# Performance work log

Hardware: AMD Instinct MI355X
Metric: run time of the kernel (lower is better)

Reference implementation:

```python
import jax, jax.numpy as jnp
import numpy as np

THRESHOLD = 0.5
EPS = 1e-8


def cos_sim(a, b):
    # a: [M, D], b: [N, D] -> [M, N] cosine similarity
    a_n = jnp.linalg.norm(a, axis=1, keepdims=True)
    b_n = jnp.linalg.norm(b, axis=1, keepdims=True)
    a_norm = a / jnp.maximum(a_n, EPS)
    b_norm = b / jnp.maximum(b_n, EPS)
    return a_norm @ b_norm.T


def setup_inputs() -> dict:
    key = jax.random.key(0)
    k1, k2, k3, k4 = jax.random.split(key, 4)
    N1, N2, FEA_FT, W_FT = 8192, 8192, 128, 64
    fea1 = jax.random.normal(k1, (N1, FEA_FT), dtype=jnp.float32)
    fea2 = jax.random.normal(k2, (N2, FEA_FT), dtype=jnp.float32)
    # xavier_uniform with relu gain sqrt(2): limit = gain * sqrt(6/(fan_in+fan_out))
    gain = float(np.sqrt(2.0))
    limit = gain * float(np.sqrt(6.0 / (FEA_FT + W_FT)))
    w1 = jax.random.uniform(k3, (FEA_FT, W_FT), minval=-limit, maxval=limit, dtype=jnp.float32)
    w2 = jax.random.uniform(k4, (FEA_FT, W_FT), minval=-limit, maxval=limit, dtype=jnp.float32)
    return {"fea1": fea1, "fea2": fea2, "w1": w1, "w2": w2}


def reference(fea1, fea2, w1, w2):
    embed1 = fea1 @ w1  # [N1, w_ft]
    embed2 = fea2 @ w2  # [N2, w_ft]
    sim_up = cos_sim(embed1, embed2)  # [N1, N2]
    sims_up = jnp.where(sim_up < THRESHOLD, jnp.zeros_like(sim_up), sim_up)
    sim_uu = cos_sim(embed1, embed1)  # [N1, N1]
    sims_uu = jnp.where(sim_uu < THRESHOLD, jnp.zeros_like(sim_uu), sim_uu)
    # Edge lists in the original are nonzero(sims_up)/nonzero(sims_uu); we return
    # the thresholded similarity matrices (jit-safe, fixed shape), stacked.
    return jnp.stack([sims_up, sims_uu], axis=0)  # [2, N, N]
```

## Files before the change

kernel.cpp:

```cpp
#include <hip/hip_runtime.h>

#define THRESH 0.5f
#define BAND   1e-3f

constexpr int N  = 8192;
constexpr int FD = 128;
constexpr int WD = 64;

typedef __attribute__((ext_vector_type(8)))  short short8;
typedef __attribute__((ext_vector_type(4)))  float f32x4;

static __device__ __forceinline__ unsigned short f2bf(float x) {
  union { float f; unsigned u; } v; v.f = x;
  unsigned r = v.u + 0x7FFFu + ((v.u >> 16) & 1u);
  return (unsigned short)(r >> 16);
}
static __device__ __forceinline__ float bf2f(unsigned short h) {
  union { unsigned u; float f; } v; v.u = (unsigned)h << 16;
  return v.f;
}

static __device__ __noinline__ float exact_dot(const float* __restrict__ a,
                                               const float* __restrict__ b) {
  float s = 0.f;
#pragma unroll 1
  for (int k = 0; k < WD; ++k) s = fmaf(a[k], b[k], s);
  return s;
}

__global__ __launch_bounds__(256) void embed_norm(
    const float* __restrict__ fea1, const float* __restrict__ fea2,
    const float* __restrict__ w1,   const float* __restrict__ w2,
    float* __restrict__ E1n, float* __restrict__ E2n,
    unsigned short* __restrict__ E1h, unsigned short* __restrict__ E1l,
    unsigned short* __restrict__ E2h, unsigned short* __restrict__ E2l) {
  const int which = blockIdx.y;
  const float* __restrict__ fea = which ? fea2 : fea1;
  const float* __restrict__ w   = which ? w2   : w1;
  float*          En = which ? E2n : E1n;
  unsigned short* Eh = which ? E2h : E1h;
  unsigned short* El = which ? E2l : E1l;

  __shared__ float wl[FD * WD];
  __shared__ float fl[32][FD];

  const int t    = threadIdx.x;
  const int row0 = blockIdx.x * 32;

#pragma unroll
  for (int i = 0; i < 8; ++i) {
    const int idx = (t + i * 256) * 4;
    *(float4*)&wl[idx] = *(const float4*)&w[idx];
  }
#pragma unroll
  for (int i = 0; i < 4; ++i) {
    const int idx = t + i * 256;
    const int r = idx >> 5;
    const int c = (idx & 31) * 4;
    *(float4*)&fl[r][c] = *(const float4*)&fea[(size_t)(row0 + r) * FD + c];
  }
  __syncthreads();

  const int wave = t >> 6, lane = t & 63;
#pragma unroll 1
  for (int rr = 0; rr < 8; ++rr) {
    const int r = wave * 8 + rr;
    float acc = 0.f;
#pragma unroll 16
    for (int k = 0; k < FD; ++k)
      acc = fmaf(fl[r][k], wl[k * WD + lane], acc);
    float ss = acc * acc;
#pragma unroll
    for (int m = 32; m >= 1; m >>= 1) ss += __shfl_xor(ss, m, 64);
    const float scale = 1.f / fmaxf(sqrtf(ss), 1e-8f);
    const float e = acc * scale;
    const size_t o = (size_t)(row0 + r) * WD + lane;
    En[o] = e;
    const unsigned short h = f2bf(e);
    Eh[o] = h;
    El[o] = f2bf(e - bf2f(h));
  }
}

__global__ __launch_bounds__(256) void sim_mfma(
    const unsigned short* __restrict__ E1h, const unsigned short* __restrict__ E1l,
    const unsigned short* __restrict__ E2h, const unsigned short* __restrict__ E2l,
    const float* __restrict__ E1n, const float* __restrict__ E2n,
    float* __restrict__ out) {
  const int bi = blockIdx.y, bj = blockIdx.x;
  const int t = threadIdx.x, w = t >> 6, lane = t & 63;
  const int wr = w >> 1, wc = w & 1;
  const int row0 = bi * 128 + wr * 64;
  const int col0 = bj * 128 + wc * 64;
  const int fr = lane & 15;
  const int fg = lane >> 4;

  short8 yh[2][4], yl[2][4];
#pragma unroll
  for (int ks = 0; ks < 2; ++ks)
#pragma unroll
    for (int ti = 0; ti < 4; ++ti) {
      const size_t r = (size_t)(row0 + ti * 16 + fr) * WD + ks * 32 + fg * 8;
      yh[ks][ti] = *(const short8*)(E1h + r);
      yl[ks][ti] = *(const short8*)(E1l + r);
    }

#pragma unroll 1
  for (int plane = 0; plane < 2; ++plane) {
    const unsigned short* __restrict__ Xh = plane ? E1h : E2h;
    const unsigned short* __restrict__ Xl = plane ? E1l : E2l;
    const float*          __restrict__ Xn = plane ? E1n : E2n;

    f32x4 acc[4][4] = {};
#pragma unroll
    for (int ks = 0; ks < 2; ++ks) {
      short8 xh[4], xl[4];
#pragma unroll
      for (int tj = 0; tj < 4; ++tj) {
        const size_t r = (size_t)(col0 + tj * 16 + fr) * WD + ks * 32 + fg * 8;
        xh[tj] = *(const short8*)(Xh + r);
        xl[tj] = *(const short8*)(Xl + r);
      }
#pragma unroll
      for (int tj = 0; tj < 4; ++tj)
#pragma unroll
        for (int ti = 0; ti < 4; ++ti) {
          acc[tj][ti] = __builtin_amdgcn_mfma_f32_16x16x32_bf16(xh[tj], yh[ks][ti], acc[tj][ti], 0, 0, 0);
          acc[tj][ti] = __builtin_amdgcn_mfma_f32_16x16x32_bf16(xh[tj], yl[ks][ti], acc[tj][ti], 0, 0, 0);
          acc[tj][ti] = __builtin_amdgcn_mfma_f32_16x16x32_bf16(xl[tj], yh[ks][ti], acc[tj][ti], 0, 0, 0);
          acc[tj][ti] = __builtin_amdgcn_mfma_f32_16x16x32_bf16(xl[tj], yl[ks][ti], acc[tj][ti], 0, 0, 0);
        }
    }

    float* __restrict__ o = out + (size_t)plane * N * N;
#pragma unroll
    for (int tj = 0; tj < 4; ++tj)
#pragma unroll
      for (int ti = 0; ti < 4; ++ti) {
        const int m  = row0 + ti * 16 + fr;
        const int nb = col0 + tj * 16 + fg * 4;
        const f32x4 v = acc[tj][ti];
        f32x4 sv;
#pragma unroll
        for (int r = 0; r < 4; ++r) {
          float val = v[r];
          if (fabsf(val - THRESH) < BAND)
            val = exact_dot(E1n + (size_t)m * WD, Xn + (size_t)(nb + r) * WD);
          sv[r] = (val < THRESH) ? 0.f : val;
        }
        __builtin_nontemporal_store(sv, (f32x4*)(o + (size_t)m * N + nb));
      }
  }
}

extern "C" void kernel_launch(void* const* d_in, const int* in_sizes, int n_in,
                              void* d_out, int out_size, void* d_ws, size_t ws_size,
                              hipStream_t stream) {
  const float* fea1 = (const float*)d_in[0];
  const float* fea2 = (const float*)d_in[1];
  const float* w1   = (const float*)d_in[2];
  const float* w2   = (const float*)d_in[3];
  float* out = (float*)d_out;

  char* ws = (char*)d_ws;
  float*          E1n = (float*)(ws);
  float*          E2n = (float*)(ws + (2u << 20));
  unsigned short* E1h = (unsigned short*)(ws + (4u << 20));
  unsigned short* E1l = (unsigned short*)(ws + (5u << 20));
  unsigned short* E2h = (unsigned short*)(ws + (6u << 20));
  unsigned short* E2l = (unsigned short*)(ws + (7u << 20));

  embed_norm<<<dim3(N / 32, 2), 256, 0, stream>>>(
      fea1, fea2, w1, w2, E1n, E2n, E1h, E1l, E2h, E2l);
  sim_mfma<<<dim3(64, 64), 256, 0, stream>>>(
      E1h, E1l, E2h, E2l, E1n, E2n, out);
}
```

Baseline: 618.8 us.

## Reload row fragments per k-step and interleave MFMA chains to cut register pressure

```diff
diff --git a/kernel.cpp b/kernel.cpp
--- a/kernel.cpp
+++ b/kernel.cpp
@@ -82,7 +82,7 @@
   }
 }
 
-__global__ __launch_bounds__(256) void sim_mfma(
+__global__ __launch_bounds__(256, 3) void sim_mfma(
     const unsigned short* __restrict__ E1h, const unsigned short* __restrict__ E1l,
     const unsigned short* __restrict__ E2h, const unsigned short* __restrict__ E2l,
     const float* __restrict__ E1n, const float* __restrict__ E2n,
@@ -95,16 +95,6 @@
   const int fr = lane & 15;
   const int fg = lane >> 4;
 
-  short8 yh[2][4], yl[2][4];
-#pragma unroll
-  for (int ks = 0; ks < 2; ++ks)
-#pragma unroll
-    for (int ti = 0; ti < 4; ++ti) {
-      const size_t r = (size_t)(row0 + ti * 16 + fr) * WD + ks * 32 + fg * 8;
-      yh[ks][ti] = *(const short8*)(E1h + r);
-      yl[ks][ti] = *(const short8*)(E1l + r);
-    }
-
 #pragma unroll 1
   for (int plane = 0; plane < 2; ++plane) {
     const unsigned short* __restrict__ Xh = plane ? E1h : E2h;
@@ -112,24 +102,39 @@
     const float*          __restrict__ Xn = plane ? E1n : E2n;
 
     f32x4 acc[4][4] = {};
+#pragma unroll 1
+    for (int ks = 0; ks < 2; ++ks) {
+      const int koff = ks * 32 + fg * 8;
+      short8 yh[4], yl[4], xh[4], xl[4];
 #pragma unroll
-    for (int ks = 0; ks < 2; ++ks) {
-      short8 xh[4], xl[4];
-#pragma unroll
-      for (int tj = 0; tj < 4; ++tj) {
-        const size_t r = (size_t)(col0 + tj * 16 + fr) * WD + ks * 32 + fg * 8;
-        xh[tj] = *(const short8*)(Xh + r);
-        xl[tj] = *(const short8*)(Xl + r);
+      for (int ti = 0; ti < 4; ++ti) {
+        const size_t ra = (size_t)(row0 + ti * 16 + fr) * WD + koff;
+        yh[ti] = *(const short8*)(E1h + ra);
+        yl[ti] = *(const short8*)(E1l + ra);
+        const size_t rb = (size_t)(col0 + ti * 16 + fr) * WD + koff;
+        xh[ti] = *(const short8*)(Xh + rb);
+        xl[ti] = *(const short8*)(Xl + rb);
       }
 #pragma unroll
       for (int tj = 0; tj < 4; ++tj)
 #pragma unroll
-        for (int ti = 0; ti < 4; ++ti) {
-          acc[tj][ti] = __builtin_amdgcn_mfma_f32_16x16x32_bf16(xh[tj], yh[ks][ti], acc[tj][ti], 0, 0, 0);
-          acc[tj][ti] = __builtin_amdgcn_mfma_f32_16x16x32_bf16(xh[tj], yl[ks][ti], acc[tj][ti], 0, 0, 0);
-          acc[tj][ti] = __builtin_amdgcn_mfma_f32_16x16x32_bf16(xl[tj], yh[ks][ti], acc[tj][ti], 0, 0, 0);
-          acc[tj][ti] = __builtin_amdgcn_mfma_f32_16x16x32_bf16(xl[tj], yl[ks][ti], acc[tj][ti], 0, 0, 0);
-        }
+        for (int ti = 0; ti < 4; ++ti)
+          acc[tj][ti] = __builtin_amdgcn_mfma_f32_16x16x32_bf16(xh[tj], yh[ti], acc[tj][ti], 0, 0, 0);
+#pragma unroll
+      for (int tj = 0; tj < 4; ++tj)
+#pragma unroll
+        for (int ti = 0; ti < 4; ++ti)
+          acc[tj][ti] = __builtin_amdgcn_mfma_f32_16x16x32_bf16(xh[tj], yl[ti], acc[tj][ti], 0, 0, 0);
+#pragma unroll
+      for (int tj = 0; tj < 4; ++tj)
+#pragma unroll
+        for (int ti = 0; ti < 4; ++ti)
+          acc[tj][ti] = __builtin_amdgcn_mfma_f32_16x16x32_bf16(xl[tj], yh[ti], acc[tj][ti], 0, 0, 0);
+#pragma unroll
+      for (int tj = 0; tj < 4; ++tj)
+#pragma unroll
+        for (int ti = 0; ti < 4; ++ti)
+          acc[tj][ti] = __builtin_amdgcn_mfma_f32_16x16x32_bf16(xl[tj], yl[ti], acc[tj][ti], 0, 0, 0);
     }
 
     float* __restrict__ o = out + (size_t)plane * N * N;
```

Measured after the change: 664.5 us. 1.07x slower.
